# Kernel tuning notes

Measured on AMD Instinct MI355X. Metric: run time of the kernel, lower is better.

## Reference

```python
import jax, jax.numpy as jnp
import numpy as np

B = 4
DIM = 512          # d_model
L = 4096           # n_tokens
D_STATE = 16
D_CONV = 4
EXPAND = 2
D_INNER = EXPAND * DIM          # 1024
DT_RANK = (DIM + 15) // 16      # ceil(dim/16) = 32
EPS = 1e-5


def setup_inputs() -> dict:
    key = jax.random.key(0)
    ks = jax.random.split(key, 8)
    s = 0.02
    A_log = jnp.log(jnp.tile(jnp.arange(1.0, D_STATE + 1.0, dtype=jnp.float32), (D_INNER, 1)))
    return {
        "x": jax.random.normal(ks[0], (B, DIM, L), jnp.float32),
        "ln_w": jnp.ones((DIM,), jnp.float32),
        "ln_b": jnp.zeros((DIM,), jnp.float32),
        "W_in": jax.random.normal(ks[1], (2 * D_INNER, DIM), jnp.float32) * s,
        "conv_w": jax.random.normal(ks[2], (D_INNER, 1, D_CONV), jnp.float32) * s,
        "conv_b": jnp.zeros((D_INNER,), jnp.float32),
        "W_xproj": jax.random.normal(ks[3], (DT_RANK + 2 * D_STATE, D_INNER), jnp.float32) * s,
        "W_dt": jax.random.normal(ks[4], (D_INNER, DT_RANK), jnp.float32) * s,
        "b_dt": jax.random.normal(ks[5], (D_INNER,), jnp.float32) * 0.1,
        "A_log": A_log,
        "D": jnp.ones((D_INNER,), jnp.float32),
        "W_out": jax.random.normal(ks[6], (DIM, D_INNER), jnp.float32) * s,
    }


def reference(x, ln_w, ln_b, W_in, conv_w, conv_b, W_xproj, W_dt, b_dt, A_log, D, W_out):
    Bsz = x.shape[0]
    # [B, d_model, L] -> [B, L, d_model]
    xt = jnp.swapaxes(x, 1, 2)
    # LayerNorm
    mu = jnp.mean(xt, axis=-1, keepdims=True)
    var = jnp.mean(jnp.square(xt - mu), axis=-1, keepdims=True)
    xn = (xt - mu) * jax.lax.rsqrt(var + EPS) * ln_w + ln_b
    # in_proj -> x, z branches
    xz = xn @ W_in.T                       # [B, L, 2*d_inner]
    xin, z = jnp.split(xz, 2, axis=-1)
    # causal depthwise conv1d (torch pads d_conv-1 both sides then truncates to L)
    xc = jnp.swapaxes(xin, 1, 2)           # [B, d_inner, L]
    xc = jax.lax.conv_general_dilated(
        xc, conv_w, window_strides=(1,), padding=[(D_CONV - 1, 0)],
        dimension_numbers=("NCH", "OIH", "NCH"), feature_group_count=D_INNER)
    xc = xc + conv_b[None, :, None]
    u = jax.nn.silu(jnp.swapaxes(xc, 1, 2))  # [B, L, d_inner]
    # input-dependent SSM parameters
    dbl = u @ W_xproj.T                    # [B, L, dt_rank + 2*d_state]
    dt = dbl[..., :DT_RANK]
    Bm = dbl[..., DT_RANK:DT_RANK + D_STATE]
    Cm = dbl[..., DT_RANK + D_STATE:]
    delta = jax.nn.softplus(dt @ W_dt.T + b_dt)  # [B, L, d_inner]
    A = -jnp.exp(A_log)                    # [d_inner, d_state]

    def step(h, inp):
        d_t, b_t, c_t, u_t = inp           # [B,di], [B,ds], [B,ds], [B,di]
        dA = jnp.exp(d_t[..., None] * A)   # [B, di, ds]
        h = dA * h + (d_t * u_t)[..., None] * b_t[:, None, :]
        y = jnp.einsum("bds,bs->bd", h, c_t)
        return h, y

    h0 = jnp.zeros((Bsz, D_INNER, D_STATE), x.dtype)
    xs = (jnp.swapaxes(delta, 0, 1), jnp.swapaxes(Bm, 0, 1),
          jnp.swapaxes(Cm, 0, 1), jnp.swapaxes(u, 0, 1))
    _, ys = jax.lax.scan(step, h0, xs)     # ys: [L, B, d_inner]
    y = jnp.swapaxes(ys, 0, 1) + u * D
    y = y * jax.nn.silu(z)
    out = y @ W_out.T                      # [B, L, d_model]
    return jnp.swapaxes(out, 1, 2)         # [B, d_model, L]
```

## Files before the change

kernel.cpp:

```cpp
#include <hip/hip_runtime.h>
#include <math.h>

#define Bsz 4
#define DIM 512
#define LEN 4096
#define DST 16
#define DIN 1024
#define NCH 64
#define CHL 64
#define LDP 72

typedef unsigned short ushort_t;
typedef unsigned int uint_t;
typedef __attribute__((ext_vector_type(8))) short short8;
typedef __attribute__((ext_vector_type(8))) unsigned short ushort8;
typedef __attribute__((ext_vector_type(8))) _Float16 half8;
typedef __attribute__((ext_vector_type(4))) float f32x4;

__device__ __forceinline__ float sigmoidf_(float x){ return 1.0f/(1.0f+__expf(-x)); }
__device__ __forceinline__ float bf2f(ushort_t u){ return __uint_as_float(((uint_t)u) << 16); }
__device__ __forceinline__ ushort_t f2bf(float f){
  uint_t x = __float_as_uint(f);
  uint_t r = (x + 0x7FFFu + ((x >> 16) & 1u)) >> 16;
  return (ushort_t)r;
}
__device__ __forceinline__ ushort_t f2h_bits(float f){
  _Float16 h = (_Float16)f;
  union { _Float16 h; ushort_t u; } v; v.h = h; return v.u;
}
__device__ __forceinline__ void gl2lds16(const void* g, void* l){
  __builtin_amdgcn_global_load_lds((const __attribute__((address_space(1))) void*)g,
                                   (__attribute__((address_space(3))) void*)l, 16, 0, 0);
}
#define POW_CHAIN(av, a1) \
  { float a2=a1*a1, a4=a2*a2, a8=a4*a4; \
    av[0]=a1; av[1]=a2; av[2]=a2*a1; av[3]=a4; \
    av[4]=a4*a1; av[5]=a4*a2; av[6]=a4*av[2]; av[7]=a8; \
    av[8]=a8*a1; av[9]=a8*a2; av[10]=a8*av[2]; av[11]=a8*a4; \
    av[12]=a8*av[4]; av[13]=a8*av[5]; av[14]=a8*av[6]; av[15]=a8*a8; }

__device__ __forceinline__ bool load_nA(const float* Alog, int d, float* nA){
  bool fast = true;
  #pragma unroll
  for(int s=0;s<DST;s++){
    float v = -__expf(Alog[d*DST+s]);
    float tgt = -(float)(s+1);
    if(fabsf(v - tgt) < 1e-4f*(float)(s+1)) v = tgt;
    else fast = false;
    nA[s] = v;
  }
  return fast;
}

__global__ __launch_bounds__(256) void ln_stats_k(const float* __restrict__ x,
                                                  float* __restrict__ mu, float* __restrict__ rs){
  int bid = blockIdx.x;
  int b = bid >> 6;
  int lg = bid & 63;
  int lane = threadIdx.x & 63;
  int g = threadIdx.x >> 6;
  int l = lg*64 + lane;
  const float* xb = x + (size_t)b*DIM*LEN + l;
  float s = 0.f, sq = 0.f;
  for(int d = g*128; d < g*128 + 128; ++d){
    float v = xb[(size_t)d*LEN];
    s += v; sq += v*v;
  }
  __shared__ float rsum[4][64], rsq[4][64];
  rsum[g][lane] = s; rsq[g][lane] = sq;
  __syncthreads();
  if(threadIdx.x < 64){
    float ts = 0.f, tq = 0.f;
    for(int gg=0; gg<4; ++gg){ ts += rsum[gg][lane]; tq += rsq[gg][lane]; }
    float m = ts * (1.0f/DIM);
    float var = tq * (1.0f/DIM) - m*m;
    mu[b*LEN + l] = m;
    rs[b*LEN + l] = rsqrtf(var + 1e-5f);
  }
}

__global__ __launch_bounds__(256) void wcvt_k(const float* __restrict__ Win,
    const float* __restrict__ Wout, const float* __restrict__ Wxp,
    ushort_t* __restrict__ Winb, ushort_t* __restrict__ Woutb, ushort_t* __restrict__ Wxpb){
  int i = blockIdx.x*256 + threadIdx.x;
  if(i < 1048576) Winb[i] = f2bf(Win[i]);
  else if(i < 1572864) Woutb[i-1048576] = f2bf(Wout[i-1048576]);
  else if(i < 1638400) Wxpb[i-1572864] = f2bf(Wxp[i-1572864]);
}

__global__ __launch_bounds__(256) void xnt_k(const float* __restrict__ x,
    const float* __restrict__ mu, const float* __restrict__ rs,
    const float* __restrict__ lnw, const float* __restrict__ lnb, ushort_t* __restrict__ xnT){
  __shared__ ushort_t t[64][72];
  int bid = blockIdx.x;
  int lt = bid & 63;
  int dt_ = (bid >> 6) & 7;
  int b = bid >> 9;
  int l0 = lt*64, d0 = dt_*64;
  int ll = threadIdx.x & 63;
  int dq = threadIdx.x >> 6;
  float mul_ = mu[b*LEN + l0 + ll], rsl = rs[b*LEN + l0 + ll];
  const float* xb = x + (size_t)b*DIM*LEN;
  #pragma unroll
  for(int i=0;i<16;i++){
    int d = d0 + dq*16 + i;
    float v = xb[(size_t)d*LEN + l0 + ll];
    t[ll][dq*16 + i] = f2bf((v - mul_)*rsl*lnw[d] + lnb[d]);
  }
  __syncthreads();
  int lr = threadIdx.x >> 2, seg = threadIdx.x & 3;
  ushort_t* dst = &xnT[(size_t)(b*LEN + l0 + lr)*DIM + d0 + seg*16];
  #pragma unroll
  for(int k=0;k<4;k++){
    ushort4 v = *(const ushort4*)&t[lr][seg*16 + k*4];
    *(ushort4*)&dst[k*4] = v;
  }
}

__global__ __launch_bounds__(256) void gemm1_mfma(const ushort_t* __restrict__ A,
    const ushort_t* __restrict__ Bw, _Float16* __restrict__ xin, ushort_t* __restrict__ sz){
  __shared__ __align__(16) ushort_t smem[2*128*LDP];
  ushort_t* As = smem;
  ushort_t* Bs = smem + 128*LDP;
  int tid = threadIdx.x;
  int wave = tid >> 6, lane = tid & 63;
  int n0 = blockIdx.x * 128;
  int m0 = blockIdx.y * 128;
  int wm = (wave >> 1) * 64, wn = (wave & 1) * 64;
  int lm = lane & 15;
  int lk = lane >> 4;
  f32x4 zero4 = {0.f,0.f,0.f,0.f};
  f32x4 acc[4][4];
  #pragma unroll
  for(int i=0;i<4;i++)
    #pragma unroll
    for(int j=0;j<4;j++) acc[i][j] = zero4;
  ushort8 ar[4], br[4];
  #pragma unroll
  for(int i=0;i<4;i++){
    int c = i*256 + tid, r = c >> 3, kc = c & 7;
    ar[i] = *(const ushort8*)&A [(size_t)(m0 + r)*512 + kc*8];
    br[i] = *(const ushort8*)&Bw[(size_t)(n0 + r)*512 + kc*8];
  }
  for(int k0=0; k0<512; k0+=64){
    __syncthreads();
    #pragma unroll
    for(int i=0;i<4;i++){
      int c = i*256 + tid, r = c >> 3, kc = c & 7;
      *(ushort8*)&As[r*LDP + kc*8] = ar[i];
      *(ushort8*)&Bs[r*LDP + kc*8] = br[i];
    }
    if(k0 + 64 < 512){
      #pragma unroll
      for(int i=0;i<4;i++){
        int c = i*256 + tid, r = c >> 3, kc = c & 7;
        ar[i] = *(const ushort8*)&A [(size_t)(m0 + r)*512 + k0 + 64 + kc*8];
        br[i] = *(const ushort8*)&Bw[(size_t)(n0 + r)*512 + k0 + 64 + kc*8];
      }
    }
    __syncthreads();
    #pragma unroll
    for(int kk=0; kk<64; kk+=32){
      short8 af[4], bf[4];
      #pragma unroll
      for(int i=0;i<4;i++){
        af[i] = *(const short8*)&As[(wm + i*16 + lm)*LDP + kk + lk*8];
        bf[i] = *(const short8*)&Bs[(wn + i*16 + lm)*LDP + kk + lk*8];
      }
      #pragma unroll
      for(int i=0;i<4;i++)
        #pragma unroll
        for(int j=0;j<4;j++)
          acc[i][j] = __builtin_amdgcn_mfma_f32_16x16x32_bf16(af[i], bf[j], acc[i][j], 0, 0, 0);
    }
  }
  __syncthreads();
  ushort_t* T = smem;
  bool is_z = (n0 >= 1024);
  #pragma unroll
  for(int i=0;i<4;i++)
    #pragma unroll
    for(int j=0;j<4;j++)
      #pragma unroll
      for(int r=0;r<4;r++){
        int ml = wm + i*16 + lk*4 + r;
        int nl = wn + j*16 + lm;
        float v = acc[i][j][r];
        T[ml*136 + nl] = is_z ? f2bf(v * sigmoidf_(v)) : f2h_bits(v);
      }
  __syncthreads();
  int rr = tid >> 4, cc = (tid & 15)*8;
  #pragma unroll
  for(int p=0;p<8;p++){
    int row = p*16 + rr;
    ushort8 v = *(const ushort8*)&T[row*136 + cc];
    if(!is_z) *(ushort8*)((ushort_t*)xin + (size_t)(m0+row)*DIN + n0 + cc) = v;
    else      *(ushort8*)&sz[(size_t)(m0+row)*DIN + (n0-1024) + cc] = v;
  }
}

__global__ __launch_bounds__(256) void conv_silu_k(const _Float16* __restrict__ xin,
    const float* __restrict__ cw, const float* __restrict__ cb, ushort_t* __restrict__ u){
  int idx = blockIdx.x*256 + threadIdx.x;
  int dg = idx & 127;
  int lc = (idx >> 7) & 511;
  int b  = idx >> 16;
  int d0 = dg*8;
  int l0 = lc*8;
  float bias[8];
  #pragma unroll
  for(int k=0;k<8;k+=4){
    float4 c4 = *(const float4*)&cb[d0+k];
    bias[k]=c4.x; bias[k+1]=c4.y; bias[k+2]=c4.z; bias[k+3]=c4.w;
  }
  float w[8][4];
  #pragma unroll
  for(int k=0;k<8;k++){
    float4 c4 = *(const float4*)&cw[(d0+k)*4];
    w[k][0]=c4.x; w[k][1]=c4.y; w[k][2]=c4.z; w[k][3]=c4.w;
  }
  const _Float16* base = xin + ((size_t)b*LEN)*DIN + d0;
  ushort_t* ub = u + ((size_t)b*LEN)*DIN + d0;
  float f0[8], f1[8], f2[8];
  if(lc > 0){
    half8 h0 = *(const half8*)&base[(size_t)(l0-3)*DIN];
    half8 h1 = *(const half8*)&base[(size_t)(l0-2)*DIN];
    half8 h2 = *(const half8*)&base[(size_t)(l0-1)*DIN];
    #pragma unroll
    for(int k=0;k<8;k++){ f0[k]=(float)h0[k]; f1[k]=(float)h1[k]; f2[k]=(float)h2[k]; }
  } else {
    #pragma unroll
    for(int k=0;k<8;k++){ f0[k]=0.f; f1[k]=0.f; f2[k]=0.f; }
  }
  #pragma unroll
  for(int t=0;t<8;t++){
    half8 xv = *(const half8*)&base[(size_t)(l0+t)*DIN];
    float f3[8];
    #pragma unroll
    for(int k=0;k<8;k++) f3[k] = (float)xv[k];
    short8 o;
    #pragma unroll
    for(int k=0;k<8;k++){
      float a = bias[k] + f0[k]*w[k][0] + f1[k]*w[k][1] + f2[k]*w[k][2] + f3[k]*w[k][3];
      float v = a * sigmoidf_(a);
      o[k] = (short)f2bf(v);
    }
    *(short8*)&ub[(size_t)(l0+t)*DIN] = o;
    #pragma unroll
    for(int k=0;k<8;k++){ f0[k]=f1[k]; f1[k]=f2[k]; f2[k]=f3[k]; }
  }
}

__global__ __launch_bounds__(256) void gemm2_mfma(const ushort_t* __restrict__ A,
    const ushort_t* __restrict__ Bw, float* __restrict__ dbl){
  __shared__ __align__(16) ushort_t As[128*64];
  __shared__ __align__(16) ushort_t Bs[64*64];
  int tid = threadIdx.x;
  int wave = tid >> 6, lane = tid & 63;
  int m0 = blockIdx.x * 128;
  int wm = (wave >> 1) * 64, wn = (wave & 1) * 32;
  int lm = lane & 15;
  int lk = lane >> 4;
  f32x4 zero4 = {0.f,0.f,0.f,0.f};
  f32x4 acc[4][2];
  #pragma unroll
  for(int i=0;i<4;i++){ acc[i][0] = zero4; acc[i][1] = zero4; }
  for(int k0=0; k0<1024; k0+=64){
    __syncthreads();
    #pragma unroll
    for(int i=0;i<4;i++){
      int c = i*256 + tid;
      int r = c >> 3, kc = c & 7;
      gl2lds16(&A[(size_t)(m0 + r)*1024 + k0 + kc*8], &As[c*8]);
    }
    #pragma unroll
    for(int i=0;i<2;i++){
      int c = i*256 + tid;
      int r = c >> 3, kc = c & 7;
      gl2lds16(&Bw[(size_t)r*1024 + k0 + kc*8], &Bs[c*8]);
    }
    __syncthreads();
    #pragma unroll
    for(int kk=0; kk<64; kk+=32){
      short8 af[4], bf[2];
      #pragma unroll
      for(int i=0;i<4;i++) af[i] = *(const short8*)&As[(wm + i*16 + lm)*64 + kk + lk*8];
      #pragma unroll
      for(int j=0;j<2;j++) bf[j] = *(const short8*)&Bs[(wn + j*16 + lm)*64 + kk + lk*8];
      #pragma unroll
      for(int i=0;i<4;i++)
        #pragma unroll
        for(int j=0;j<2;j++)
          acc[i][j] = __builtin_amdgcn_mfma_f32_16x16x32_bf16(af[i], bf[j], acc[i][j], 0, 0, 0);
    }
  }
  #pragma unroll
  for(int i=0;i<4;i++)
    #pragma unroll
    for(int j=0;j<2;j++)
      #pragma unroll
      for(int r=0;r<4;r++){
        int m = m0 + wm + i*16 + lk*4 + r;
        int n = wn + j*16 + lm;
        dbl[(size_t)m*64 + n] = acc[i][j][r];
      }
}

__global__ __launch_bounds__(256,4) void deltag_k(const float* __restrict__ dbl,
    const float* __restrict__ Wdt, const float* __restrict__ bdt,
    _Float16* __restrict__ dF){
  __shared__ __align__(16) float dts[64*32];
  int bid = blockIdx.x;
  int d0 = (bid & 3) * 256;
  int m0 = (bid >> 2) * 64;
  int tid = threadIdx.x;
  const f32x4* src4 = (const f32x4*)(dbl + (size_t)m0*64);
  f32x4* dst4 = (f32x4*)dts;
  for(int i=tid; i<64*8; i+=256){
    int row = i >> 3, q = i & 7;
    dst4[i] = src4[row*16 + q];
  }
  int d = d0 + tid;
  float w[32];
  #pragma unroll
  for(int k=0;k<32;k+=4){
    float4 t4 = *(const float4*)&Wdt[d*32+k];
    w[k]=t4.x; w[k+1]=t4.y; w[k+2]=t4.z; w[k+3]=t4.w;
  }
  float bd = bdt[d];
  __syncthreads();
  for(int m=0;m<64;m++){
    const float* row = dts + m*32;
    float dtv = bd;
    #pragma unroll
    for(int k=0;k<32;k+=4){
      f32x4 q = *(const f32x4*)&row[k];
      dtv += q.x*w[k] + q.y*w[k+1] + q.z*w[k+2] + q.w*w[k+3];
    }
    float dv = dtv > 15.f ? dtv : __logf(1.f + __expf(dtv));
    dF[(size_t)(m0+m)*DIN + d] = (_Float16)dv;
  }
}

__global__ __launch_bounds__(256,4) void scanA_k(const ushort_t* __restrict__ u,
    const float* __restrict__ dbl, const float* __restrict__ Alog,
    const _Float16* __restrict__ dF,
    float* __restrict__ E, float* __restrict__ cum){
  __shared__ __align__(16) float dch[CHL*16];
  int bid = blockIdx.x;
  int c = bid & (NCH-1);
  int dblk = (bid >> 6) & 3;
  int b = bid >> 8;
  int d = dblk*256 + threadIdx.x;
  const f32x4* src = (const f32x4*)(dbl + ((size_t)b*LEN + c*CHL)*64);
  f32x4* dst4 = (f32x4*)dch;
  for(int i=threadIdx.x; i<CHL*4; i+=256){
    int t = i >> 2, q = i & 3;
    dst4[i] = src[t*16 + 8 + q];
  }
  float nA[DST];
  bool fast = load_nA(Alog, d, nA);
  float Es[DST];
  #pragma unroll
  for(int s=0;s<DST;s++) Es[s] = 0.f;
  float cumD = 0.f;
  __syncthreads();
  const ushort_t*  uu = u  + ((size_t)b*LEN + c*CHL)*DIN + d;
  const _Float16*  pd = dF + ((size_t)b*LEN + c*CHL)*DIN + d;
  if(fast){
    for(int t=0;t<CHL;++t){
      float dv = (float)pd[(size_t)t*DIN];
      float uv = bf2f(uu[(size_t)t*DIN]);
      float du = dv*uv;
      cumD += dv;
      float a1 = __expf(-dv);
      float av[DST];
      POW_CHAIN(av, a1);
      const f32x4* r4 = (const f32x4*)(dch + t*16);
      f32x4 B0=r4[0], B1=r4[1], B2=r4[2], B3=r4[3];
      Es[0]=av[0]*Es[0]+du*B0.x;  Es[1]=av[1]*Es[1]+du*B0.y;
      Es[2]=av[2]*Es[2]+du*B0.z;  Es[3]=av[3]*Es[3]+du*B0.w;
      Es[4]=av[4]*Es[4]+du*B1.x;  Es[5]=av[5]*Es[5]+du*B1.y;
      Es[6]=av[6]*Es[6]+du*B1.z;  Es[7]=av[7]*Es[7]+du*B1.w;
      Es[8]=av[8]*Es[8]+du*B2.x;  Es[9]=av[9]*Es[9]+du*B2.y;
      Es[10]=av[10]*Es[10]+du*B2.z; Es[11]=av[11]*Es[11]+du*B2.w;
      Es[12]=av[12]*Es[12]+du*B3.x; Es[13]=av[13]*Es[13]+du*B3.y;
      Es[14]=av[14]*Es[14]+du*B3.z; Es[15]=av[15]*Es[15]+du*B3.w;
    }
  } else {
    for(int t=0;t<CHL;++t){
      float dv = (float)pd[(size_t)t*DIN];
      float uv = bf2f(uu[(size_t)t*DIN]);
      float du = dv*uv;
      cumD += dv;
      const float* row = dch + t*16;
      #pragma unroll
      for(int s=0;s<DST;s++){
        float a = __expf(dv*nA[s]);
        Es[s] = a*Es[s] + du*row[s];
      }
    }
  }
  size_t o = (size_t)(b*NCH + c)*DST*DIN + d;
  #pragma unroll
  for(int s=0;s<DST;s++) E[o + (size_t)s*DIN] = Es[s];
  cum[(size_t)(b*NCH + c)*DIN + d] = cumD;
}

__global__ __launch_bounds__(256) void scanB_k(const float* __restrict__ cum,
    const float* __restrict__ Alog, float* __restrict__ E){
  int g = blockIdx.x*256 + threadIdx.x;
  int d = g & 1023;
  int s = (g >> 10) & 15;
  int b = g >> 14;
  float v = -__expf(Alog[d*DST + s]);
  float tgt = -(float)(s+1);
  float nA = (fabsf(v - tgt) < 1e-4f*(float)(s+1)) ? tgt : v;
  float h = 0.f;
  for(int c=0;c<NCH;c++){
    float p = __expf(cum[(size_t)(b*NCH + c)*DIN + d] * nA);
    size_t o = (size_t)((b*NCH + c)*DST + s)*DIN + d;
    float e = E[o];
    E[o] = h;
    h = p*h + e;
  }
}

__global__ __launch_bounds__(256,4) void scanC_k(ushort_t* __restrict__ u,
    const float* __restrict__ dbl, const float* __restrict__ Alog,
    const float* __restrict__ Hs, const float* __restrict__ Dp, const ushort_t* __restrict__ sz,
    const _Float16* __restrict__ dF){
  __shared__ __align__(16) float dch[CHL*32];
  int bid = blockIdx.x;
  int c = bid & (NCH-1);
  int dblk = (bid >> 6) & 3;
  int b = bid >> 8;
  int d = dblk*256 + threadIdx.x;
  const f32x4* src = (const f32x4*)(dbl + ((size_t)b*LEN + c*CHL)*64);
  f32x4* dst4 = (f32x4*)dch;
  for(int i=threadIdx.x; i<CHL*8; i+=256){
    int t = i >> 3, q = i & 7;
    dst4[i] = src[t*16 + 8 + q];
  }
  float nA[DST];
  bool fast = load_nA(Alog, d, nA);
  float h[DST];
  size_t ho = (size_t)(b*NCH + c)*DST*DIN + d;
  #pragma unroll
  for(int s=0;s<DST;s++) h[s] = Hs[ho + (size_t)s*DIN];
  float Dv = Dp[d];
  __syncthreads();
  ushort_t* uu = u + ((size_t)b*LEN + c*CHL)*DIN + d;
  const ushort_t* zz = sz + ((size_t)b*LEN + c*CHL)*DIN + d;
  const _Float16* pd = dF + ((size_t)b*LEN + c*CHL)*DIN + d;
  if(fast){
    for(int t=0;t<CHL;++t){
      float dv = (float)pd[(size_t)t*DIN];
      float uv = bf2f(uu[(size_t)t*DIN]);
      float du = dv*uv;
      float a1 = __expf(-dv);
      float av[DST];
      POW_CHAIN(av, a1);
      const f32x4* r4 = (const f32x4*)(dch + t*32);
      f32x4 B0=r4[0], B1=r4[1], B2=r4[2], B3=r4[3];
      f32x4 C0=r4[4], C1=r4[5], C2=r4[6], C3=r4[7];
      float y0, y1, y2, y3;
      h[0]=av[0]*h[0]+du*B0.x;  h[1]=av[1]*h[1]+du*B0.y;
      h[2]=av[2]*h[2]+du*B0.z;  h[3]=av[3]*h[3]+du*B0.w;
      y0 = h[0]*C0.x + h[1]*C0.y; y1 = h[2]*C0.z + h[3]*C0.w;
      h[4]=av[4]*h[4]+du*B1.x;  h[5]=av[5]*h[5]+du*B1.y;
      h[6]=av[6]*h[6]+du*B1.z;  h[7]=av[7]*h[7]+du*B1.w;
      y2 = h[4]*C1.x + h[5]*C1.y; y3 = h[6]*C1.z + h[7]*C1.w;
      h[8]=av[8]*h[8]+du*B2.x;  h[9]=av[9]*h[9]+du*B2.y;
      h[10]=av[10]*h[10]+du*B2.z; h[11]=av[11]*h[11]+du*B2.w;
      y0 += h[8]*C2.x + h[9]*C2.y; y1 += h[10]*C2.z + h[11]*C2.w;
      h[12]=av[12]*h[12]+du*B3.x; h[13]=av[13]*h[13]+du*B3.y;
      h[14]=av[14]*h[14]+du*B3.z; h[15]=av[15]*h[15]+du*B3.w;
      y2 += h[12]*C3.x + h[13]*C3.y; y3 += h[14]*C3.z + h[15]*C3.w;
      float y = (y0+y1) + (y2+y3) + uv*Dv;
      y *= bf2f(zz[(size_t)t*DIN]);
      uu[(size_t)t*DIN] = f2bf(y);
    }
  } else {
    for(int t=0;t<CHL;++t){
      float dv = (float)pd[(size_t)t*DIN];
      float uv = bf2f(uu[(size_t)t*DIN]);
      float du = dv*uv;
      const float* row = dch + t*32;
      float y = 0.f;
      #pragma unroll
      for(int s=0;s<DST;s++){
        float a = __expf(dv*nA[s]);
        h[s] = a*h[s] + du*row[s];
        y += h[s]*row[16+s];
      }
      y += uv*Dv;
      y *= bf2f(zz[(size_t)t*DIN]);
      uu[(size_t)t*DIN] = f2bf(y);
    }
  }
}

__global__ __launch_bounds__(256) void gemm4_mfma(const ushort_t* __restrict__ A,
    const ushort_t* __restrict__ Bw, float* __restrict__ out){
  __shared__ __align__(16) ushort_t smem[2*128*LDP];
  ushort_t* As = smem;
  ushort_t* Bs = smem + 128*LDP;
  int tid = threadIdx.x;
  int wave = tid >> 6, lane = tid & 63;
  int n0 = blockIdx.x * 128;
  int m0 = blockIdx.y * 128;
  int wm = (wave >> 1) * 64, wn = (wave & 1) * 64;
  int lm = lane & 15;
  int lk = lane >> 4;
  f32x4 zero4 = {0.f,0.f,0.f,0.f};
  f32x4 acc[4][4];
  #pragma unroll
  for(int i=0;i<4;i++)
    #pragma unroll
    for(int j=0;j<4;j++) acc[i][j] = zero4;
  ushort8 ar[4], br[4];
  #pragma unroll
  for(int i=0;i<4;i++){
    int c = i*256 + tid, r = c >> 3, kc = c & 7;
    ar[i] = *(const ushort8*)&A [(size_t)(m0 + r)*1024 + kc*8];
    br[i] = *(const ushort8*)&Bw[(size_t)(n0 + r)*1024 + kc*8];
  }
  for(int k0=0; k0<1024; k0+=64){
    __syncthreads();
    #pragma unroll
    for(int i=0;i<4;i++){
      int c = i*256 + tid, r = c >> 3, kc = c & 7;
      *(ushort8*)&As[r*LDP + kc*8] = ar[i];
      *(ushort8*)&Bs[r*LDP + kc*8] = br[i];
    }
    if(k0 + 64 < 1024){
      #pragma unroll
      for(int i=0;i<4;i++){
        int c = i*256 + tid, r = c >> 3, kc = c & 7;
        ar[i] = *(const ushort8*)&A [(size_t)(m0 + r)*1024 + k0 + 64 + kc*8];
        br[i] = *(const ushort8*)&Bw[(size_t)(n0 + r)*1024 + k0 + 64 + kc*8];
      }
    }
    __syncthreads();
    #pragma unroll
    for(int kk=0; kk<64; kk+=32){
      short8 af[4], bf[4];
      #pragma unroll
      for(int i=0;i<4;i++){
        af[i] = *(const short8*)&As[(wm + i*16 + lm)*LDP + kk + lk*8];
        bf[i] = *(const short8*)&Bs[(wn + i*16 + lm)*LDP + kk + lk*8];
      }
      #pragma unroll
      for(int i=0;i<4;i++)
        #pragma unroll
        for(int j=0;j<4;j++)
          acc[i][j] = __builtin_amdgcn_mfma_f32_16x16x32_bf16(af[i], bf[j], acc[i][j], 0, 0, 0);
    }
  }
  float* T = (float*)smem;
  int b = m0 >> 12, l0 = m0 & 4095;
  for(int g=0; g<4; ++g){
    __syncthreads();
    if((g >> 1) == (wave & 1)){
      int jg = g & 1;
      #pragma unroll
      for(int j2=0;j2<2;j2++){
        int j = jg*2 + j2;
        #pragma unroll
        for(int i=0;i<4;i++)
          #pragma unroll
          for(int r=0;r<4;r++){
            int ml = wm + i*16 + lk*4 + r;
            int nl = wn + j*16 + lm - g*32;
            T[nl*132 + ml] = acc[i][j][r];
          }
      }
    }
    __syncthreads();
    int nl = tid >> 3, seg = tid & 7;
    float* dst = &out[((size_t)b*DIM + n0 + g*32 + nl)*LEN + l0 + seg*16];
    #pragma unroll
    for(int k=0;k<4;k++){
      float4 v = *(const float4*)&T[nl*132 + seg*16 + k*4];
      *(float4*)&dst[k*4] = v;
    }
  }
}

extern "C" void kernel_launch(void* const* d_in, const int* in_sizes, int n_in,
                              void* d_out, int out_size, void* d_ws, size_t ws_size,
                              hipStream_t stream) {
  const float* x    = (const float*)d_in[0];
  const float* lnw  = (const float*)d_in[1];
  const float* lnb  = (const float*)d_in[2];
  const float* Win  = (const float*)d_in[3];
  const float* cw   = (const float*)d_in[4];
  const float* cb   = (const float*)d_in[5];
  const float* Wxp  = (const float*)d_in[6];
  const float* Wdt  = (const float*)d_in[7];
  const float* bdt  = (const float*)d_in[8];
  const float* Alog = (const float*)d_in[9];
  const float* Dp   = (const float*)d_in[10];
  const float* Wout = (const float*)d_in[11];
  float* out = (float*)d_out;
  float* ws  = (float*)d_ws;

  float*    mu   = ws;
  float*    rs   = ws + 16384;
  _Float16* xin  = (_Float16*)(ws + 32768);
  _Float16* dF   = (_Float16*)(ws + 32768);
  float*    E    = ws + 32768 + 8388608;
  float*    cum  = ws + 32768 + 12582912;
  ushort_t* sz   = (ushort_t*)(ws + 32768 + 16777216);
  ushort_t* u    = (ushort_t*)(ws + 32768 + 16777216 + 8388608);
  ushort_t* xnT  = (ushort_t*)(ws + 32768 + 16777216 + 16777216);
  float*    dbl  = (float*)xnT;
  ushort_t* Winb = (ushort_t*)(ws + 32768 + 16777216 + 16777216 + 4194304);
  ushort_t* Woutb= Winb + 1048576;
  ushort_t* Wxpb = Woutb + 524288;

  hipLaunchKernelGGL(ln_stats_k, dim3(256),     dim3(256), 0, stream, x, mu, rs);
  hipLaunchKernelGGL(wcvt_k,     dim3(6400),    dim3(256), 0, stream, Win, Wout, Wxp, Winb, Woutb, Wxpb);
  hipLaunchKernelGGL(xnt_k,      dim3(2048),    dim3(256), 0, stream, x, mu, rs, lnw, lnb, xnT);
  hipLaunchKernelGGL(gemm1_mfma, dim3(16,128),  dim3(256), 0, stream, xnT, Winb, xin, sz);
  hipLaunchKernelGGL(conv_silu_k,dim3(1024),    dim3(256), 0, stream, xin, cw, cb, u);
  hipLaunchKernelGGL(gemm2_mfma, dim3(128),     dim3(256), 0, stream, u, Wxpb, dbl);
  hipLaunchKernelGGL(deltag_k,   dim3(1024),    dim3(256), 0, stream, dbl, Wdt, bdt, dF);
  hipLaunchKernelGGL(scanA_k,    dim3(1024),    dim3(256), 0, stream, u, dbl, Alog, dF, E, cum);
  hipLaunchKernelGGL(scanB_k,    dim3(256),     dim3(256), 0, stream, cum, Alog, E);
  hipLaunchKernelGGL(scanC_k,    dim3(1024),    dim3(256), 0, stream, u, dbl, Alog, E, Dp, sz, dF);
  hipLaunchKernelGGL(gemm4_mfma, dim3(4,128),   dim3(256), 0, stream, u, Woutb, out);
}
```

Measured before the change: 365.1 us.

## Load GEMM tiles directly global-to-LDS and remap blocks for locality

In the two MFMA GEMM kernels, the register-staged prefetch of A and B tiles is replaced with direct global-to-LDS 16-byte loads (gl2lds16). The LDS row stride drops from the padded 72 to an unpadded 64. Block indices are also permuted so that consecutive workgroups spread across tiles, aiming for better L2 reuse across XCDs. This removes register pressure and VGPR-to-LDS store instructions, but it loses the software prefetch overlap and may add LDS bank conflicts on the fragment reads now that padding is gone.

New measurement: 378.3 us. +3.6%, slower.

```diff
diff --git a/kernel.cpp b/kernel.cpp
--- a/kernel.cpp
+++ b/kernel.cpp
@@ -121,11 +121,13 @@
     const ushort_t* __restrict__ Bw, _Float16* __restrict__ xin, ushort_t* __restrict__ sz){
   __shared__ __align__(16) ushort_t smem[2*128*LDP];
   ushort_t* As = smem;
-  ushort_t* Bs = smem + 128*LDP;
+  ushort_t* Bs = smem + 128*64;
   int tid = threadIdx.x;
   int wave = tid >> 6, lane = tid & 63;
-  int n0 = blockIdx.x * 128;
-  int m0 = blockIdx.y * 128;
+  int flat = blockIdx.y * 16 + blockIdx.x;
+  int orig = (flat & 7) * 256 + (flat >> 3);
+  int n0 = (orig & 15) * 128;
+  int m0 = (orig >> 4) * 128;
   int wm = (wave >> 1) * 64, wn = (wave & 1) * 64;
   int lm = lane & 15;
   int lk = lane >> 4;
@@ -135,28 +137,17 @@
   for(int i=0;i<4;i++)
     #pragma unroll
     for(int j=0;j<4;j++) acc[i][j] = zero4;
-  ushort8 ar[4], br[4];
-  #pragma unroll
-  for(int i=0;i<4;i++){
-    int c = i*256 + tid, r = c >> 3, kc = c & 7;
-    ar[i] = *(const ushort8*)&A [(size_t)(m0 + r)*512 + kc*8];
-    br[i] = *(const ushort8*)&Bw[(size_t)(n0 + r)*512 + kc*8];
-  }
   for(int k0=0; k0<512; k0+=64){
     __syncthreads();
     #pragma unroll
     for(int i=0;i<4;i++){
       int c = i*256 + tid, r = c >> 3, kc = c & 7;
-      *(ushort8*)&As[r*LDP + kc*8] = ar[i];
-      *(ushort8*)&Bs[r*LDP + kc*8] = br[i];
-    }
-    if(k0 + 64 < 512){
-      #pragma unroll
-      for(int i=0;i<4;i++){
-        int c = i*256 + tid, r = c >> 3, kc = c & 7;
-        ar[i] = *(const ushort8*)&A [(size_t)(m0 + r)*512 + k0 + 64 + kc*8];
-        br[i] = *(const ushort8*)&Bw[(size_t)(n0 + r)*512 + k0 + 64 + kc*8];
-      }
+      gl2lds16(&A[(size_t)(m0 + r)*512 + k0 + kc*8], &As[c*8]);
+    }
+    #pragma unroll
+    for(int i=0;i<4;i++){
+      int c = i*256 + tid, r = c >> 3, kc = c & 7;
+      gl2lds16(&Bw[(size_t)(n0 + r)*512 + k0 + kc*8], &Bs[c*8]);
     }
     __syncthreads();
     #pragma unroll
@@ -164,8 +155,8 @@
       short8 af[4], bf[4];
       #pragma unroll
       for(int i=0;i<4;i++){
-        af[i] = *(const short8*)&As[(wm + i*16 + lm)*LDP + kk + lk*8];
-        bf[i] = *(const short8*)&Bs[(wn + i*16 + lm)*LDP + kk + lk*8];
+        af[i] = *(const short8*)&As[(wm + i*16 + lm)*64 + kk + lk*8];
+        bf[i] = *(const short8*)&Bs[(wn + i*16 + lm)*64 + kk + lk*8];
       }
       #pragma unroll
       for(int i=0;i<4;i++)
@@ -505,11 +496,13 @@
     const ushort_t* __restrict__ Bw, float* __restrict__ out){
   __shared__ __align__(16) ushort_t smem[2*128*LDP];
   ushort_t* As = smem;
-  ushort_t* Bs = smem + 128*LDP;
+  ushort_t* Bs = smem + 128*64;
   int tid = threadIdx.x;
   int wave = tid >> 6, lane = tid & 63;
-  int n0 = blockIdx.x * 128;
-  int m0 = blockIdx.y * 128;
+  int flat = blockIdx.y * 4 + blockIdx.x;
+  int orig = (flat & 7) * 64 + (flat >> 3);
+  int n0 = (orig & 3) * 128;
+  int m0 = (orig >> 2) * 128;
   int wm = (wave >> 1) * 64, wn = (wave & 1) * 64;
   int lm = lane & 15;
   int lk = lane >> 4;
@@ -519,28 +512,17 @@
   for(int i=0;i<4;i++)
     #pragma unroll
     for(int j=0;j<4;j++) acc[i][j] = zero4;
-  ushort8 ar[4], br[4];
-  #pragma unroll
-  for(int i=0;i<4;i++){
-    int c = i*256 + tid, r = c >> 3, kc = c & 7;
-    ar[i] = *(const ushort8*)&A [(size_t)(m0 + r)*1024 + kc*8];
-    br[i] = *(const ushort8*)&Bw[(size_t)(n0 + r)*1024 + kc*8];
-  }
   for(int k0=0; k0<1024; k0+=64){
     __syncthreads();
     #pragma unroll
     for(int i=0;i<4;i++){
       int c = i*256 + tid, r = c >> 3, kc = c & 7;
-      *(ushort8*)&As[r*LDP + kc*8] = ar[i];
-      *(ushort8*)&Bs[r*LDP + kc*8] = br[i];
-    }
-    if(k0 + 64 < 1024){
-      #pragma unroll
-      for(int i=0;i<4;i++){
-        int c = i*256 + tid, r = c >> 3, kc = c & 7;
-        ar[i] = *(const ushort8*)&A [(size_t)(m0 + r)*1024 + k0 + 64 + kc*8];
-        br[i] = *(const ushort8*)&Bw[(size_t)(n0 + r)*1024 + k0 + 64 + kc*8];
-      }
+      gl2lds16(&A[(size_t)(m0 + r)*1024 + k0 + kc*8], &As[c*8]);
+    }
+    #pragma unroll
+    for(int i=0;i<4;i++){
+      int c = i*256 + tid, r = c >> 3, kc = c & 7;
+      gl2lds16(&Bw[(size_t)(n0 + r)*1024 + k0 + kc*8], &Bs[c*8]);
     }
     __syncthreads();
     #pragma unroll
@@ -548,8 +530,8 @@
       short8 af[4], bf[4];
       #pragma unroll
       for(int i=0;i<4;i++){
-        af[i] = *(const short8*)&As[(wm + i*16 + lm)*LDP + kk + lk*8];
-        bf[i] = *(const short8*)&Bs[(wn + i*16 + lm)*LDP + kk + lk*8];
+        af[i] = *(const short8*)&As[(wm + i*16 + lm)*64 + kk + lk*8];
+        bf[i] = *(const short8*)&Bs[(wn + i*16 + lm)*64 + kk + lk*8];
       }
       #pragma unroll
       for(int i=0;i<4;i++)
```
